# Performance work log

Hardware: AMD Instinct MI355X
Metric: run time of the kernel (lower is better)

The kernel has to match this reference:

```python
import jax, jax.numpy as jnp
import numpy as np

H = 64  # hidden_dim


def _lstm_layer(x_seq, w_ih, w_hh, b_ih, b_hh):
    """Single PyTorch-convention LSTM layer, batch_first input [B,S,F] -> [B,S,H]."""
    B = x_seq.shape[0]
    # precompute input-to-gate projections for all timesteps: [B,S,4H]
    xg = jnp.einsum('bsf,gf->bsg', x_seq, w_ih) + b_ih + b_hh

    def step(carry, xt):
        h, c = carry
        gates = xt + h @ w_hh.T  # [B,4H], gate order i,f,g,o
        i, f, g, o = jnp.split(gates, 4, axis=-1)
        c = jax.nn.sigmoid(f) * c + jax.nn.sigmoid(i) * jnp.tanh(g)
        h = jax.nn.sigmoid(o) * jnp.tanh(c)
        return (h, c), h

    init = (jnp.zeros((B, H), x_seq.dtype), jnp.zeros((B, H), x_seq.dtype))
    (_, _), hs = jax.lax.scan(step, init, jnp.swapaxes(xg, 0, 1))  # [S,B,H]
    return jnp.swapaxes(hs, 0, 1)


def setup_inputs() -> dict:
    key = jax.random.key(0)
    ks = jax.random.split(key, 20)
    s = 0.1  # small init scale to avoid gate saturation
    d = {
        'x': jax.random.normal(ks[0], (4096, 256, 5), jnp.float32),
        'w_ih0': s * jax.random.normal(ks[1], (256, 5), jnp.float32),
        'w_hh0': s * jax.random.normal(ks[2], (256, 64), jnp.float32),
        'b_ih0': s * jax.random.normal(ks[3], (256,), jnp.float32),
        'b_hh0': s * jax.random.normal(ks[4], (256,), jnp.float32),
        'w_ih1': s * jax.random.normal(ks[5], (256, 64), jnp.float32),
        'w_hh1': s * jax.random.normal(ks[6], (256, 64), jnp.float32),
        'b_ih1': s * jax.random.normal(ks[7], (256,), jnp.float32),
        'b_hh1': s * jax.random.normal(ks[8], (256,), jnp.float32),
        'eng_w1': s * jax.random.normal(ks[9], (16, 64), jnp.float32),
        'eng_b1': s * jax.random.normal(ks[10], (16,), jnp.float32),
        'eng_w2': s * jax.random.normal(ks[11], (1, 16), jnp.float32),
        'eng_b2': s * jax.random.normal(ks[12], (1,), jnp.float32),
        'prop_w1': s * jax.random.normal(ks[13], (16, 64), jnp.float32),
        'prop_b1': s * jax.random.normal(ks[14], (16,), jnp.float32),
        'prop_w2': s * jax.random.normal(ks[15], (1, 16), jnp.float32),
        'prop_b2': s * jax.random.normal(ks[16], (1,), jnp.float32),
        'seg_w': s * jax.random.normal(ks[17], (5, 64), jnp.float32),
        'seg_b': s * jax.random.normal(ks[18], (5,), jnp.float32),
    }
    return d


def reference(x, w_ih0, w_hh0, b_ih0, b_hh0, w_ih1, w_hh1, b_ih1, b_hh1,
              eng_w1, eng_b1, eng_w2, eng_b2,
              prop_w1, prop_b1, prop_w2, prop_b2, seg_w, seg_b):
    # 2-layer LSTM (inference: dropout = identity)
    h1 = _lstm_layer(x, w_ih0, w_hh0, b_ih0, b_hh0)   # [B,S,64]
    h2 = _lstm_layer(h1, w_ih1, w_hh1, b_ih1, b_hh1)  # [B,S,64]
    last = h2[:, -1, :]                                # [B,64]

    def mlp_head(w1, b1, w2, b2):
        hdn = jax.nn.relu(last @ w1.T + b1)
        return jax.nn.sigmoid(hdn @ w2.T + b2)[:, 0]   # squeeze(-1)

    engagement = mlp_head(eng_w1, eng_b1, eng_w2, eng_b2)   # [B]
    propensity = mlp_head(prop_w1, prop_b1, prop_w2, prop_b2)  # [B]
    segment_logits = last @ seg_w.T + seg_b                  # [B,5]
    return engagement, propensity, segment_logits
```

## Files before the change

### kernel.cpp

```cpp
#include <hip/hip_runtime.h>

typedef __attribute__((ext_vector_type(8))) short short8_t;
typedef __attribute__((ext_vector_type(4))) float f32x4;
typedef __attribute__((ext_vector_type(2))) float f32x2;

#define SEQ  256
#define HID  64
#define FIN  5
#define BB   16
#define TPB  1024
#define BTOT 4096

#define OFF_W0HI 0
#define OFF_W1HI (64*1024)
#define OFF_W2HI (128*1024)
#define OFF_WX   (192*1024)
#define OFF_B1   (208*1024)

#define NL2E 1.44269504088896f
#if __has_builtin(__builtin_amdgcn_exp2f)
#define EXP2(v) __builtin_amdgcn_exp2f(v)
#else
#define EXP2(v) __expf((v) * 0.6931471805599453f)
#endif

#define MFMA(A, B, C) __builtin_amdgcn_mfma_f32_16x16x32_bf16((A), (B), (C), 0, 0, 0)

__device__ __forceinline__ float rcp_(float v) { return __builtin_amdgcn_rcpf(v); }
__device__ __forceinline__ unsigned short bf16rtn(float v) {
    unsigned int u = __float_as_uint(v);
    u += 0x7fffu + ((u >> 16) & 1u);
    return (unsigned short)(u >> 16);
}
__device__ __forceinline__ float bf16tof(unsigned short h) {
    return __uint_as_float(((unsigned int)h) << 16);
}
__device__ __forceinline__ float sigf(float v) { return rcp_(1.0f + EXP2(v * -NL2E)); }

__global__ void prep_kernel(const float* __restrict__ wih0, const float* __restrict__ whh0,
                            const float* __restrict__ bih0, const float* __restrict__ bhh0,
                            const float* __restrict__ wih1, const float* __restrict__ whh1,
                            const float* __restrict__ bih1, const float* __restrict__ bhh1,
                            unsigned char* __restrict__ ws) {
    int idx = blockIdx.x * blockDim.x + threadIdx.x;
    if (idx < 3 * 16384) {
        int mat = idx / 16384, e = idx % 16384;
        int tk   = e >> 9;
        int lane = (e >> 3) & 63;
        int i    = e & 7;
        int c = 16 * (tk >> 1) + (lane & 15);
        int k = (tk & 1) * 32 + (lane >> 4) * 8 + i;
        int gate = c & 3;
        int row = gate * 64 + (c >> 2);
        float scale = (gate == 2) ? (-2.0f * NL2E) : -NL2E;
        const float* W = (mat == 0) ? whh0 : (mat == 1) ? whh1 : wih1;
        float v = W[row * HID + k] * scale;
        int bhiOff = (mat == 0) ? OFF_W0HI : (mat == 1) ? OFF_W1HI : OFF_W2HI;
        ((unsigned short*)(ws + bhiOff))[e] = bf16rtn(v);
    } else if (idx < 3 * 16384 + 8192) {
        int e = idx - 3 * 16384;
        int w = e >> 9, r2 = e & 511;
        int lane = r2 >> 3, i = r2 & 7;
        int c = 16 * w + (lane & 15);
        int k = (lane >> 4) * 8 + i;
        int gate = c & 3;
        int row = gate * 64 + (c >> 2);
        float scale = (gate == 2) ? (-2.0f * NL2E) : -NL2E;
        unsigned short outv = 0;
        if (k < 15) {
            float v = wih0[row * FIN + (k % 5)] * scale;
            unsigned int vb = __float_as_uint(v);
            if (k < 10) outv = (unsigned short)(vb >> 16);
            else        outv = bf16rtn(v - __uint_as_float(vb & 0xffff0000u));
        } else if (k == 15 || k == 16) {
            float bv = (bih0[row] + bhh0[row]) * scale;
            unsigned int vb = __float_as_uint(bv);
            if (k == 15) outv = (unsigned short)(vb >> 16);
            else         outv = bf16rtn(bv - __uint_as_float(vb & 0xffff0000u));
        }
        ((unsigned short*)(ws + OFF_WX))[e] = outv;
    }
    if (idx < 256) {
        int gate = idx & 3;
        int row = gate * 64 + (idx >> 2);
        float scale = (gate == 2) ? (-2.0f * NL2E) : -NL2E;
        ((float*)(ws + OFF_B1))[idx] = (bih1[row] + bhh1[row]) * scale;
    }
}

__global__ __launch_bounds__(TPB, 4)
void lstm_fused_kernel(const float* __restrict__ x, const unsigned char* __restrict__ ws,
                       const float* __restrict__ ew1, const float* __restrict__ eb1,
                       const float* __restrict__ ew2, const float* __restrict__ eb2,
                       const float* __restrict__ pw1, const float* __restrict__ pb1,
                       const float* __restrict__ pw2, const float* __restrict__ pb2,
                       const float* __restrict__ sw,  const float* __restrict__ sb,
                       float* __restrict__ out) {
    __shared__ __attribute__((aligned(16))) unsigned short VS0[2][2][64][8];
    __shared__ __attribute__((aligned(16))) unsigned short VS1[2][2][64][8];
    __shared__ __attribute__((aligned(16))) unsigned short XF[4][64][8];
    __shared__ float HS[2][16][17];

    const int tid  = threadIdx.x;
    const int lane = tid & 63;
    const int w    = tid >> 6;
    const int b    = lane & 15;
    const int g    = lane >> 4;
    const int b0g  = blockIdx.x * BB;
    const bool isL0 = (w >= 8);
    const int wt   = w & 7;

    for (int i = tid; i < 2 * 2 * 64 * 8; i += TPB) {
        (&VS0[0][0][0][0])[i] = 0; (&VS1[0][0][0][0])[i] = 0;
    }
    for (int i = tid; i < 4 * 64 * 8; i += TPB) (&XF[0][0][0])[i] = 0;

    short8_t Fa[2][2], Fb[2][2], FX2[2];
    f32x4 biasA, biasB;
    if (!isL0) {
        #pragma unroll
        for (int s = 0; s < 2; ++s)
            #pragma unroll
            for (int ks = 0; ks < 2; ++ks) {
                const int fo = (((wt + 8 * s) * 2 + ks) * 64 + lane) * 16;
                Fa[s][ks] = *(const short8_t*)(ws + OFF_W1HI + fo);
                Fb[s][ks] = *(const short8_t*)(ws + OFF_W2HI + fo);
            }
        #pragma unroll
        for (int r = 0; r < 4; ++r) {
            biasA[r] = ((const float*)(ws + OFF_B1))[16 * wt + 4 * g + r];
            biasB[r] = ((const float*)(ws + OFF_B1))[16 * (wt + 8) + 4 * g + r];
        }
    } else {
        #pragma unroll
        for (int s = 0; s < 2; ++s) {
            #pragma unroll
            for (int ks = 0; ks < 2; ++ks) {
                const int fo = (((wt + 8 * s) * 2 + ks) * 64 + lane) * 16;
                Fa[s][ks] = *(const short8_t*)(ws + OFF_W0HI + fo);
            }
            FX2[s] = *(const short8_t*)(ws + OFF_WX + ((wt + 8 * s) * 64 + lane) * 16);
        }
        biasA[0] = 0.f; biasA[1] = 0.f; biasA[2] = 0.f; biasA[3] = 0.f;
        biasB = biasA;
    }

    const int strow  = ((wt >> 1) & 3) * 16 + b;
    const int stelem = 4 * (wt & 1) + g;
    unsigned short* sta = isL0 ? &VS0[0][0][strow][stelem] : &VS1[0][0][strow][stelem];
    unsigned short* stb = sta + 512;

    f32x2 cc2 = {0.f, 0.f};
    short8_t xfc;

#define PACK_X(SLOT, RL) {                                                          \
    unsigned int u0 = __float_as_uint(bx0), u1 = __float_as_uint(bx1),              \
                 u2 = __float_as_uint(bx2), u3 = __float_as_uint(bx3),              \
                 u4 = __float_as_uint(bx4);                                         \
    unsigned int h0 = u0 >> 16, h1 = u1 >> 16, h2 = u2 >> 16,                       \
                 h3 = u3 >> 16, h4 = u4 >> 16;                                      \
    unsigned int l0 = bf16rtn(bx0 - __uint_as_float(u0 & 0xffff0000u));             \
    unsigned int l1 = bf16rtn(bx1 - __uint_as_float(u1 & 0xffff0000u));             \
    unsigned int l2 = bf16rtn(bx2 - __uint_as_float(u2 & 0xffff0000u));             \
    unsigned int l3 = bf16rtn(bx3 - __uint_as_float(u3 & 0xffff0000u));             \
    unsigned int l4 = bf16rtn(bx4 - __uint_as_float(u4 & 0xffff0000u));             \
    uint4 cc0, cc1;                                                                 \
    cc0.x = h0 | (h1 << 16); cc0.y = h2 | (h3 << 16);                               \
    cc0.z = h4 | (l0 << 16); cc0.w = l1 | (l2 << 16);                               \
    cc1.x = l3 | (l4 << 16); cc1.y = h0 | (h1 << 16);                               \
    cc1.z = h2 | (h3 << 16); cc1.w = h4 | (0x3F80u << 16);                          \
    *(uint4*)&XF[SLOT][0 * 16 + (RL)][0] = cc0;                                     \
    *(uint4*)&XF[SLOT][1 * 16 + (RL)][0] = cc1;                                     \
}

#define GATES2(av0, av1, hv2) {                                                     \
    f32x2 e1 = { EXP2(av0[0]), EXP2(av1[0]) };                                      \
    f32x2 e2 = { EXP2(av0[1]), EXP2(av1[1]) };                                      \
    f32x2 e3 = { EXP2(av0[2]), EXP2(av1[2]) };                                      \
    f32x2 e4 = { EXP2(av0[3]), EXP2(av1[3]) };                                      \
    f32x2 one = { 1.0f, 1.0f };                                                     \
    f32x2 A  = one + e2;                                                            \
    f32x2 B  = (one + e1) * (one + e3);                                             \
    f32x2 num = cc2 * B + (one - e3) * A;                                           \
    f32x2 ab = A * B;                                                               \
    f32x2 rab = { rcp_(ab[0]), rcp_(ab[1]) };                                       \
    cc2 = num * rab;                                                                \
    f32x2 arg5 = cc2 * (-2.0f * NL2E);                                              \
    f32x2 e5 = { EXP2(arg5[0]), EXP2(arg5[1]) };                                    \
    f32x2 d2 = (one + e4) * (one + e5);                                             \
    f32x2 rd = { rcp_(d2[0]), rcp_(d2[1]) };                                        \
    hv2 = (one - e5) * rd;                                                          \
}

    __syncthreads();
    if (tid < 64) {
        int d = tid >> 4, bb = tid & 15;
        const float* xp_ = x + (size_t)(b0g + bb) * (SEQ * FIN) + d * FIN;
        float bx0 = xp_[0], bx1 = xp_[1], bx2 = xp_[2], bx3 = xp_[3], bx4 = xp_[4];
        PACK_X(d, bb)
        XF[d][2 * 16 + bb][0] = 0x3F80;
    }
    __syncthreads();

    if (isL0) {
        short8_t xf0 = *(const short8_t*)&XF[0][lane][0];
        f32x4 a0 = MFMA(FX2[0], xf0, biasA);
        f32x4 a1 = MFMA(FX2[1], xf0, biasB);
        f32x2 hv2;
        GATES2(a0, a1, hv2)
        unsigned int pk_;
        asm("v_cvt_pk_bf16_f32 %0, %1, %2" : "=v"(pk_) : "v"(hv2[0]), "v"(hv2[1]));
        sta[1 * 1024] = (unsigned short)pk_;
        stb[1 * 1024] = (unsigned short)(pk_ >> 16);
        xfc = *(const short8_t*)&XF[1][lane][0];
    }

#define ITER(P, R, QEXPR, BEN) {                                                        \
    __syncthreads();                                                                    \
    if (!isL0) {                                                                        \
        short8_t h20 = *(const short8_t*)&VS1[P][0][lane][0];                           \
        short8_t h21 = *(const short8_t*)&VS1[P][1][lane][0];                           \
        short8_t h10 = *(const short8_t*)&VS0[P ^ 1][0][lane][0];                       \
        short8_t h11 = *(const short8_t*)&VS0[P ^ 1][1][lane][0];                       \
        __builtin_amdgcn_s_setprio(1);                                                  \
        f32x4 d0 = MFMA(Fa[0][0], h20, biasA);                                          \
        f32x4 d1 = MFMA(Fa[1][0], h20, biasB);                                          \
        d0 = MFMA(Fa[0][1], h21, d0); d1 = MFMA(Fa[1][1], h21, d1);                     \
        d0 = MFMA(Fb[0][0], h10, d0); d1 = MFMA(Fb[1][0], h10, d1);                     \
        d0 = MFMA(Fb[0][1], h11, d0); d1 = MFMA(Fb[1][1], h11, d1);                     \
        __builtin_amdgcn_s_setprio(0);                                                  \
        f32x2 hv2;                                                                      \
        GATES2(d0, d1, hv2)                                                             \
        unsigned int pk_;                                                               \
        asm("v_cvt_pk_bf16_f32 %0, %1, %2" : "=v"(pk_) : "v"(hv2[0]), "v"(hv2[1]));     \
        sta[(P ^ 1) * 1024] = (unsigned short)pk_;                                      \
        stb[(P ^ 1) * 1024] = (unsigned short)(pk_ >> 16);                              \
    } else {                                                                            \
        const int IDX_ = 4 * (QEXPR) + (R);                                             \
        const bool bw_ = (BEN) && (w == 8 + (IDX_ & 7));                                \
        float bx0, bx1, bx2, bx3, bx4;                                                  \
        if (bw_ && lane < 16) {                                                         \
            const float* xp_ = x + (size_t)(b0g + lane) * (SEQ * FIN)                   \
                                 + (IDX_ + 4) * FIN;                                    \
            bx0 = xp_[0]; bx1 = xp_[1]; bx2 = xp_[2]; bx3 = xp_[3]; bx4 = xp_[4];       \
        }                                                                               \
        short8_t h10 = *(const short8_t*)&VS0[P ^ 1][0][lane][0];                       \
        short8_t h11 = *(const short8_t*)&VS0[P ^ 1][1][lane][0];                       \
        __builtin_amdgcn_s_setprio(1);                                                  \
        f32x4 a0 = MFMA(FX2[0], xfc, biasA);                                            \
        f32x4 a1 = MFMA(FX2[1], xfc, biasB);                                            \
        a0 = MFMA(Fa[0][0], h10, a0); a1 = MFMA(Fa[1][0], h10, a1);                     \
        a0 = MFMA(Fa[0][1], h11, a0); a1 = MFMA(Fa[1][1], h11, a1);                     \
        __builtin_amdgcn_s_setprio(0);                                                  \
        f32x2 hv2;                                                                      \
        GATES2(a0, a1, hv2)                                                             \
        unsigned int pk_;                                                               \
        asm("v_cvt_pk_bf16_f32 %0, %1, %2" : "=v"(pk_) : "v"(hv2[0]), "v"(hv2[1]));     \
        sta[P * 1024] = (unsigned short)pk_;                                            \
        stb[P * 1024] = (unsigned short)(pk_ >> 16);                                    \
        if (bw_ && lane < 16) { PACK_X((R), lane) }                                     \
        xfc = *(const short8_t*)&XF[((R) + 2) & 3][lane][0];                            \
    }                                                                                   \
}

    for (int q = 0; q < 63; ++q) {
        ITER(0, 0, q, 1)
        ITER(1, 1, q, 1)
        ITER(0, 2, q, 1)
        ITER(1, 3, q, 1)
    }
    ITER(0, 0, 63, 0)
    ITER(1, 1, 63, 0)
    ITER(0, 2, 63, 0)
    ITER(1, 3, 63, 0)
#undef ITER
#undef GATES2
#undef PACK_X

    __syncthreads();
    if (tid < 256) {
        int hb_ = tid >> 4, hi_ = tid & 15;
        float ae = eb1[hi_], ap = pb1[hi_];
        for (int j = 0; j < HID; ++j) {
            float h = bf16tof(VS1[0][j >> 5][((j >> 3) & 3) * 16 + hb_][j & 7]);
            ae += h * ew1[hi_ * HID + j];
            ap += h * pw1[hi_ * HID + j];
        }
        HS[0][hb_][hi_] = fmaxf(ae, 0.0f);
        HS[1][hb_][hi_] = fmaxf(ap, 0.0f);
    }
    if (tid >= 256 && tid < 256 + 80) {
        int t2 = tid - 256, sbb = t2 / 5, ss = t2 % 5;
        float a = sb[ss];
        for (int j = 0; j < HID; ++j)
            a += bf16tof(VS1[0][j >> 5][((j >> 3) & 3) * 16 + sbb][j & 7]) * sw[ss * HID + j];
        out[2 * BTOT + (size_t)(b0g + sbb) * 5 + ss] = a;
    }
    __syncthreads();
    if (tid < BB) {
        float eo = eb2[0], po = pb2[0];
        #pragma unroll
        for (int i2 = 0; i2 < 16; ++i2) {
            eo += HS[0][tid][i2] * ew2[i2];
            po += HS[1][tid][i2] * pw2[i2];
        }
        out[b0g + tid]        = sigf(eo);
        out[BTOT + b0g + tid] = sigf(po);
    }
}

extern "C" void kernel_launch(void* const* d_in, const int* in_sizes, int n_in,
                              void* d_out, int out_size, void* d_ws, size_t ws_size,
                              hipStream_t stream) {
    const float* x     = (const float*)d_in[0];
    const float* w_ih0 = (const float*)d_in[1];
    const float* w_hh0 = (const float*)d_in[2];
    const float* b_ih0 = (const float*)d_in[3];
    const float* b_hh0 = (const float*)d_in[4];
    const float* w_ih1 = (const float*)d_in[5];
    const float* w_hh1 = (const float*)d_in[6];
    const float* b_ih1 = (const float*)d_in[7];
    const float* b_hh1 = (const float*)d_in[8];
    const float* ew1 = (const float*)d_in[9];
    const float* eb1 = (const float*)d_in[10];
    const float* ew2 = (const float*)d_in[11];
    const float* eb2 = (const float*)d_in[12];
    const float* pw1 = (const float*)d_in[13];
    const float* pb1 = (const float*)d_in[14];
    const float* pw2 = (const float*)d_in[15];
    const float* pb2 = (const float*)d_in[16];
    const float* sw  = (const float*)d_in[17];
    const float* sb  = (const float*)d_in[18];
    float* out = (float*)d_out;
    unsigned char* ws = (unsigned char*)d_ws;

    hipLaunchKernelGGL(prep_kernel, dim3(224), dim3(256), 0, stream,
                       w_ih0, w_hh0, b_ih0, b_hh0, w_ih1, w_hh1, b_ih1, b_hh1, ws);
    hipLaunchKernelGGL(lstm_fused_kernel, dim3(BTOT / BB), dim3(TPB), 0, stream,
                       x, ws, ew1, eb1, ew2, eb2, pw1, pb1, pw2, pb2, sw, sb, out);
}
```

Baseline: 175.6 us.

## Halve block to 512 threads with four gate tiles per wave

Cuts the LSTM block from 16 waves to 8, so each wave now computes four 16-row gate tiles instead of two and carries two cell-state pairs. Each wave issues more MFMAs and gate math per timestep, while fewer waves take part in the per-step barrier and in sharing LDS. This trades per-wave instruction-level parallelism against parallelism across waves. It also raises register pressure, since weight fragments double to 16 or 20 short8 per lane.

```diff
diff --git a/kernel.cpp b/kernel.cpp
--- a/kernel.cpp
+++ b/kernel.cpp
@@ -8,7 +8,7 @@
 #define HID  64
 #define FIN  5
 #define BB   16
-#define TPB  1024
+#define TPB  512
 #define BTOT 4096
 
 #define OFF_W0HI 0
@@ -88,7 +88,7 @@
     }
 }
 
-__global__ __launch_bounds__(TPB, 4)
+__global__ __launch_bounds__(TPB, 2)
 void lstm_fused_kernel(const float* __restrict__ x, const unsigned char* __restrict__ ws,
                        const float* __restrict__ ew1, const float* __restrict__ eb1,
                        const float* __restrict__ ew2, const float* __restrict__ eb2,
@@ -107,50 +107,54 @@
     const int b    = lane & 15;
     const int g    = lane >> 4;
     const int b0g  = blockIdx.x * BB;
-    const bool isL0 = (w >= 8);
-    const int wt   = w & 7;
+    const bool isL0 = (w >= 4);
+    const int wt   = w & 3;
 
     for (int i = tid; i < 2 * 2 * 64 * 8; i += TPB) {
         (&VS0[0][0][0][0])[i] = 0; (&VS1[0][0][0][0])[i] = 0;
     }
     for (int i = tid; i < 4 * 64 * 8; i += TPB) (&XF[0][0][0])[i] = 0;
 
-    short8_t Fa[2][2], Fb[2][2], FX2[2];
-    f32x4 biasA, biasB;
+    short8_t Fa[4][2], Fb[4][2], FX4[4];
+    f32x4 biasT0, biasT1, biasT2, biasT3;
     if (!isL0) {
         #pragma unroll
-        for (int s = 0; s < 2; ++s)
+        for (int s = 0; s < 4; ++s)
             #pragma unroll
             for (int ks = 0; ks < 2; ++ks) {
-                const int fo = (((wt + 8 * s) * 2 + ks) * 64 + lane) * 16;
+                const int fo = (((wt + 4 * s) * 2 + ks) * 64 + lane) * 16;
                 Fa[s][ks] = *(const short8_t*)(ws + OFF_W1HI + fo);
                 Fb[s][ks] = *(const short8_t*)(ws + OFF_W2HI + fo);
             }
         #pragma unroll
         for (int r = 0; r < 4; ++r) {
-            biasA[r] = ((const float*)(ws + OFF_B1))[16 * wt + 4 * g + r];
-            biasB[r] = ((const float*)(ws + OFF_B1))[16 * (wt + 8) + 4 * g + r];
+            biasT0[r] = ((const float*)(ws + OFF_B1))[16 * wt + 4 * g + r];
+            biasT1[r] = ((const float*)(ws + OFF_B1))[16 * (wt + 4) + 4 * g + r];
+            biasT2[r] = ((const float*)(ws + OFF_B1))[16 * (wt + 8) + 4 * g + r];
+            biasT3[r] = ((const float*)(ws + OFF_B1))[16 * (wt + 12) + 4 * g + r];
         }
     } else {
         #pragma unroll
-        for (int s = 0; s < 2; ++s) {
+        for (int s = 0; s < 4; ++s) {
             #pragma unroll
             for (int ks = 0; ks < 2; ++ks) {
-                const int fo = (((wt + 8 * s) * 2 + ks) * 64 + lane) * 16;
+                const int fo = (((wt + 4 * s) * 2 + ks) * 64 + lane) * 16;
                 Fa[s][ks] = *(const short8_t*)(ws + OFF_W0HI + fo);
             }
-            FX2[s] = *(const short8_t*)(ws + OFF_WX + ((wt + 8 * s) * 64 + lane) * 16);
-        }
-        biasA[0] = 0.f; biasA[1] = 0.f; biasA[2] = 0.f; biasA[3] = 0.f;
-        biasB = biasA;
-    }
-
-    const int strow  = ((wt >> 1) & 3) * 16 + b;
-    const int stelem = 4 * (wt & 1) + g;
-    unsigned short* sta = isL0 ? &VS0[0][0][strow][stelem] : &VS1[0][0][strow][stelem];
-    unsigned short* stb = sta + 512;
-
-    f32x2 cc2 = {0.f, 0.f};
+            FX4[s] = *(const short8_t*)(ws + OFF_WX + ((wt + 4 * s) * 64 + lane) * 16);
+        }
+        biasT0[0] = 0.f; biasT0[1] = 0.f; biasT0[2] = 0.f; biasT0[3] = 0.f;
+        biasT1 = biasT0; biasT2 = biasT0; biasT3 = biasT0;
+    }
+
+    const int off0_ = ((wt >> 1) * 16 + b) * 8 + 4 * (wt & 1) + g;
+    unsigned short* base_ = isL0 ? &VS0[0][0][0][0] : &VS1[0][0][0][0];
+    unsigned short* st0 = base_ + off0_;
+    unsigned short* st1 = base_ + off0_ + 256;
+    unsigned short* st2 = base_ + off0_ + 512;
+    unsigned short* st3 = base_ + off0_ + 768;
+
+    f32x2 ccA = {0.f, 0.f}, ccB = {0.f, 0.f};
     short8_t xfc;
 
 #define PACK_X(SLOT, RL) {                                                          \
@@ -173,7 +177,7 @@
     *(uint4*)&XF[SLOT][1 * 16 + (RL)][0] = cc1;                                     \
 }
 
-#define GATES2(av0, av1, hv2) {                                                     \
+#define GATES2(av0, av1, CC, hv2) {                                                 \
     f32x2 e1 = { EXP2(av0[0]), EXP2(av1[0]) };                                      \
     f32x2 e2 = { EXP2(av0[1]), EXP2(av1[1]) };                                      \
     f32x2 e3 = { EXP2(av0[2]), EXP2(av1[2]) };                                      \
@@ -181,11 +185,11 @@
     f32x2 one = { 1.0f, 1.0f };                                                     \
     f32x2 A  = one + e2;                                                            \
     f32x2 B  = (one + e1) * (one + e3);                                             \
-    f32x2 num = cc2 * B + (one - e3) * A;                                           \
+    f32x2 num = CC * B + (one - e3) * A;                                            \
     f32x2 ab = A * B;                                                               \
     f32x2 rab = { rcp_(ab[0]), rcp_(ab[1]) };                                       \
-    cc2 = num * rab;                                                                \
-    f32x2 arg5 = cc2 * (-2.0f * NL2E);                                              \
+    CC = num * rab;                                                                 \
+    f32x2 arg5 = CC * (-2.0f * NL2E);                                               \
     f32x2 e5 = { EXP2(arg5[0]), EXP2(arg5[1]) };                                    \
     f32x2 d2 = (one + e4) * (one + e5);                                             \
     f32x2 rd = { rcp_(d2[0]), rcp_(d2[1]) };                                        \
@@ -204,14 +208,20 @@
 
     if (isL0) {
         short8_t xf0 = *(const short8_t*)&XF[0][lane][0];
-        f32x4 a0 = MFMA(FX2[0], xf0, biasA);
-        f32x4 a1 = MFMA(FX2[1], xf0, biasB);
-        f32x2 hv2;
-        GATES2(a0, a1, hv2)
-        unsigned int pk_;
-        asm("v_cvt_pk_bf16_f32 %0, %1, %2" : "=v"(pk_) : "v"(hv2[0]), "v"(hv2[1]));
-        sta[1 * 1024] = (unsigned short)pk_;
-        stb[1 * 1024] = (unsigned short)(pk_ >> 16);
+        f32x4 a0 = MFMA(FX4[0], xf0, biasT0);
+        f32x4 a1 = MFMA(FX4[1], xf0, biasT1);
+        f32x4 a2 = MFMA(FX4[2], xf0, biasT2);
+        f32x4 a3 = MFMA(FX4[3], xf0, biasT3);
+        f32x2 hvA, hvB;
+        GATES2(a0, a1, ccA, hvA)
+        GATES2(a2, a3, ccB, hvB)
+        unsigned int pk1, pk2;
+        asm("v_cvt_pk_bf16_f32 %0, %1, %2" : "=v"(pk1) : "v"(hvA[0]), "v"(hvA[1]));
+        asm("v_cvt_pk_bf16_f32 %0, %1, %2" : "=v"(pk2) : "v"(hvB[0]), "v"(hvB[1]));
+        st0[1024] = (unsigned short)pk1;
+        st1[1024] = (unsigned short)(pk1 >> 16);
+        st2[1024] = (unsigned short)pk2;
+        st3[1024] = (unsigned short)(pk2 >> 16);
         xfc = *(const short8_t*)&XF[1][lane][0];
     }
 
@@ -223,21 +233,30 @@
         short8_t h10 = *(const short8_t*)&VS0[P ^ 1][0][lane][0];                       \
         short8_t h11 = *(const short8_t*)&VS0[P ^ 1][1][lane][0];                       \
         __builtin_amdgcn_s_setprio(1);                                                  \
-        f32x4 d0 = MFMA(Fa[0][0], h20, biasA);                                          \
-        f32x4 d1 = MFMA(Fa[1][0], h20, biasB);                                          \
+        f32x4 d0 = MFMA(Fa[0][0], h20, biasT0);                                         \
+        f32x4 d1 = MFMA(Fa[1][0], h20, biasT1);                                         \
+        f32x4 d2 = MFMA(Fa[2][0], h20, biasT2);                                         \
+        f32x4 d3 = MFMA(Fa[3][0], h20, biasT3);                                         \
         d0 = MFMA(Fa[0][1], h21, d0); d1 = MFMA(Fa[1][1], h21, d1);                     \
+        d2 = MFMA(Fa[2][1], h21, d2); d3 = MFMA(Fa[3][1], h21, d3);                     \
         d0 = MFMA(Fb[0][0], h10, d0); d1 = MFMA(Fb[1][0], h10, d1);                     \
+        d2 = MFMA(Fb[2][0], h10, d2); d3 = MFMA(Fb[3][0], h10, d3);                     \
         d0 = MFMA(Fb[0][1], h11, d0); d1 = MFMA(Fb[1][1], h11, d1);                     \
+        d2 = MFMA(Fb[2][1], h11, d2); d3 = MFMA(Fb[3][1], h11, d3);                     \
         __builtin_amdgcn_s_setprio(0);                                                  \
-        f32x2 hv2;                                                                      \
-        GATES2(d0, d1, hv2)                                                             \
-        unsigned int pk_;                                                               \
-        asm("v_cvt_pk_bf16_f32 %0, %1, %2" : "=v"(pk_) : "v"(hv2[0]), "v"(hv2[1]));     \
-        sta[(P ^ 1) * 1024] = (unsigned short)pk_;                                      \
-        stb[(P ^ 1) * 1024] = (unsigned short)(pk_ >> 16);                              \
+        f32x2 hvA, hvB;                                                                 \
+        GATES2(d0, d1, ccA, hvA)                                                        \
+        GATES2(d2, d3, ccB, hvB)                                                        \
+        unsigned int pk1, pk2;                                                          \
+        asm("v_cvt_pk_bf16_f32 %0, %1, %2" : "=v"(pk1) : "v"(hvA[0]), "v"(hvA[1]));     \
+        asm("v_cvt_pk_bf16_f32 %0, %1, %2" : "=v"(pk2) : "v"(hvB[0]), "v"(hvB[1]));     \
+        st0[(P ^ 1) * 1024] = (unsigned short)pk1;                                      \
+        st1[(P ^ 1) * 1024] = (unsigned short)(pk1 >> 16);                              \
+        st2[(P ^ 1) * 1024] = (unsigned short)pk2;                                      \
+        st3[(P ^ 1) * 1024] = (unsigned short)(pk2 >> 16);                              \
     } else {                                                                            \
         const int IDX_ = 4 * (QEXPR) + (R);                                             \
-        const bool bw_ = (BEN) && (w == 8 + (IDX_ & 7));                                \
+        const bool bw_ = (BEN) && (w == 4 + (R));                                       \
         float bx0, bx1, bx2, bx3, bx4;                                                  \
         if (bw_ && lane < 16) {                                                         \
             const float* xp_ = x + (size_t)(b0g + lane) * (SEQ * FIN)                   \
@@ -247,17 +266,25 @@
         short8_t h10 = *(const short8_t*)&VS0[P ^ 1][0][lane][0];                       \
         short8_t h11 = *(const short8_t*)&VS0[P ^ 1][1][lane][0];                       \
         __builtin_amdgcn_s_setprio(1);                                                  \
-        f32x4 a0 = MFMA(FX2[0], xfc, biasA);                                            \
-        f32x4 a1 = MFMA(FX2[1], xfc, biasB);                                            \
+        f32x4 a0 = MFMA(FX4[0], xfc, biasT0);                                           \
+        f32x4 a1 = MFMA(FX4[1], xfc, biasT1);                                           \
+        f32x4 a2 = MFMA(FX4[2], xfc, biasT2);                                           \
+        f32x4 a3 = MFMA(FX4[3], xfc, biasT3);                                           \
         a0 = MFMA(Fa[0][0], h10, a0); a1 = MFMA(Fa[1][0], h10, a1);                     \
+        a2 = MFMA(Fa[2][0], h10, a2); a3 = MFMA(Fa[3][0], h10, a3);                     \
         a0 = MFMA(Fa[0][1], h11, a0); a1 = MFMA(Fa[1][1], h11, a1);                     \
+        a2 = MFMA(Fa[2][1], h11, a2); a3 = MFMA(Fa[3][1], h11, a3);                     \
         __builtin_amdgcn_s_setprio(0);                                                  \
-        f32x2 hv2;                                                                      \
-        GATES2(a0, a1, hv2)                                                             \
-        unsigned int pk_;                                                               \
-        asm("v_cvt_pk_bf16_f32 %0, %1, %2" : "=v"(pk_) : "v"(hv2[0]), "v"(hv2[1]));     \
-        sta[P * 1024] = (unsigned short)pk_;                                            \
-        stb[P * 1024] = (unsigned short)(pk_ >> 16);                                    \
+        f32x2 hvA, hvB;                                                                 \
+        GATES2(a0, a1, ccA, hvA)                                                        \
+        GATES2(a2, a3, ccB, hvB)                                                        \
+        unsigned int pk1, pk2;                                                          \
+        asm("v_cvt_pk_bf16_f32 %0, %1, %2" : "=v"(pk1) : "v"(hvA[0]), "v"(hvA[1]));     \
+        asm("v_cvt_pk_bf16_f32 %0, %1, %2" : "=v"(pk2) : "v"(hvB[0]), "v"(hvB[1]));     \
+        st0[P * 1024] = (unsigned short)pk1;                                            \
+        st1[P * 1024] = (unsigned short)(pk1 >> 16);                                    \
+        st2[P * 1024] = (unsigned short)pk2;                                            \
+        st3[P * 1024] = (unsigned short)(pk2 >> 16);                                    \
         if (bw_ && lane < 16) { PACK_X((R), lane) }                                     \
         xfc = *(const short8_t*)&XF[((R) + 2) & 3][lane][0];                            \
     }                                                                                   \
```

Result: slower. 185.4 us (+5.6%).
